# Optimization experiments

Measured on AMD Instinct MI355X. Metric: run time of the kernel, lower is better.

Reference implementation:

```python
import jax, jax.numpy as jnp
import numpy as np

B, N_C, Y_DIM = 8, 2048, 8
GRID_RES = 128
GRID_MIN, GRID_MAX = -1.0, 1.0
SIGMA0 = 0.1


def _make_grid_points():
    x = jnp.linspace(GRID_MIN, GRID_MAX, GRID_RES, dtype=jnp.float32)
    y = jnp.linspace(GRID_MIN, GRID_MAX, GRID_RES, dtype=jnp.float32)
    gy, gx = jnp.meshgrid(y, x, indexing='ij')
    return jnp.stack([gx, gy], axis=-1).reshape(1, -1, 2)  # (1, R*R, 2)


def setup_inputs() -> dict:
    key = jax.random.key(0)
    k1, k2 = jax.random.split(key)
    x_c = jax.random.uniform(k1, (B, N_C, 2), dtype=jnp.float32, minval=GRID_MIN, maxval=GRID_MAX)
    y_c = jax.random.normal(k2, (B, N_C, Y_DIM), dtype=jnp.float32)
    grid_points = _make_grid_points()
    sigma = jnp.asarray(SIGMA0, dtype=jnp.float32)
    return {"x_c": x_c, "y_c": y_c, "grid_points": grid_points, "sigma": sigma}


def reference(x_c, y_c, grid_points, sigma):
    g = grid_points[0]                                    # (M, 2)
    xn = jnp.sum(x_c * x_c, axis=-1)                      # (B, N)
    gn = jnp.sum(g * g, axis=-1)                          # (M,)
    cross = jnp.einsum('bnd,md->bnm', x_c, g)             # (B, N, M)
    d2 = xn[:, :, None] + gn[None, None, :] - 2.0 * cross # (B, N, M)
    weights = jnp.exp(-0.5 * d2 / (sigma * sigma))        # (B, N, M)
    density = jnp.sum(weights, axis=1)                    # (B, M)
    signal = jnp.einsum('bny,bnm->bym', y_c, weights)     # (B, Y, M)
    normalized = signal / (density[:, None, :] + 1e-5)
    out = jnp.concatenate([density[:, None, :], normalized], axis=1)  # (B, 1+Y, M)
    return out.reshape(x_c.shape[0], -1, GRID_RES, GRID_RES)
```

## Files before the change

### kernel.cpp

```cpp
#include <hip/hip_runtime.h>


typedef float  f32x4 __attribute__((ext_vector_type(4)));
typedef __fp16 half8  __attribute__((ext_vector_type(8)));
typedef __fp16 half2t __attribute__((ext_vector_type(2)));

constexpr int B_  = 8;
constexpr int NC  = 2048;
constexpr int M_  = 128 * 128;
constexpr int BLK = 1024;
constexpr int KW  = 128;
constexpr int LDHY = NC + 8;

constexpr int OFF_SXT = 0;
constexpr int OFF_SYT = OFF_SXT + NC * 4;
constexpr int OFF_SYS = OFF_SYT + NC * 4;
constexpr int OFF_SG  = OFF_SYS + 8 * LDHY * 2;
constexpr int SLOT_F  = 2 * 9 * 256;
constexpr int POOL_B  = 8 * SLOT_F * 4;

__global__ __launch_bounds__(BLK) void rbf_sep(
    const float* __restrict__ x_c,
    const float* __restrict__ y_c,
    const float* __restrict__ gp,
    const float* __restrict__ sigma_p,
    float* __restrict__ out)
{
    __shared__ __align__(16) char pool[POOL_B];
    float*  sxt = (float*)(pool + OFF_SXT);
    float*  syt = (float*)(pool + OFF_SYT);
    __fp16* sys = (__fp16*)(pool + OFF_SYS);
    float*  sg  = (float*)(pool + OFF_SG);

    const int tid  = (int)threadIdx.x;
    const int lane = tid & 63;
    const int w    = tid >> 6;
    const int q    = lane >> 4;
    const int cl   = lane & 15;

    const int bid = blockIdx.x;
    const int b   = bid >> 5;
    const int myg = (bid >> 3) & 3;
    const int mxg = bid & 7;
    const int my0 = myg * 32;
    const int mx0 = mxg * 16;

    const float sigma = sigma_p[0];
    const float s = __builtin_sqrtf(0.72134752044448170f) / sigma;

    if (tid < 32)      sg[tid] = s * gp[(my0 + tid) * 256 + 1];
    else if (tid < 48) sg[tid] = s * gp[(mx0 + (tid - 32)) * 2];

    const float2* xb = (const float2*)x_c + (size_t)b * NC;
    const float4* yb = (const float4*)y_c + (size_t)b * NC * 2;
    for (int it = tid; it < NC; it += BLK) {
        const float2 v = xb[it];
        sxt[it] = s * v.x;
        syt[it] = s * v.y;
        const float4 y0 = yb[(size_t)it * 2];
        const float4 y1 = yb[(size_t)it * 2 + 1];
        __fp16* yw = sys + it;
        yw[0 * LDHY] = (__fp16)y0.x;
        yw[1 * LDHY] = (__fp16)y0.y;
        yw[2 * LDHY] = (__fp16)y0.z;
        yw[3 * LDHY] = (__fp16)y0.w;
        yw[4 * LDHY] = (__fp16)y1.x;
        yw[5 * LDHY] = (__fp16)y1.y;
        yw[6 * LDHY] = (__fp16)y1.z;
        yw[7 * LDHY] = (__fp16)y1.w;
    }
    __syncthreads();

    const float sgy0 = sg[cl];
    const float sgy1 = sg[16 + cl];
    const float sgxr = sg[32 + cl];

    f32x4 acc[2][9];
#pragma unroll
    for (int t = 0; t < 2; ++t)
#pragma unroll
        for (int c = 0; c < 9; ++c) acc[t][c] = (f32x4)0.0f;

    const int kbase = w * KW;
#pragma unroll 2
    for (int ks = 0; ks < KW / 32; ++ks) {
        const int kq = kbase + ks * 32 + q * 8;

        const f32x4 ya0 = *(const f32x4*)(syt + kq);
        const f32x4 ya1 = *(const f32x4*)(syt + kq + 4);
        const f32x4 xa0 = *(const f32x4*)(sxt + kq);
        const f32x4 xa1 = *(const f32x4*)(sxt + kq + 4);

        const f32x4 y0e0 = ya0 - sgy0, y0e1 = ya1 - sgy0;
        const f32x4 y0m0 = y0e0 * y0e0, y0m1 = y0e1 * y0e1;
        const half2t p00 = __builtin_amdgcn_cvt_pkrtz(
            __builtin_amdgcn_exp2f(-y0m0.x), __builtin_amdgcn_exp2f(-y0m0.y));
        const half2t p01 = __builtin_amdgcn_cvt_pkrtz(
            __builtin_amdgcn_exp2f(-y0m0.z), __builtin_amdgcn_exp2f(-y0m0.w));
        const half2t p02 = __builtin_amdgcn_cvt_pkrtz(
            __builtin_amdgcn_exp2f(-y0m1.x), __builtin_amdgcn_exp2f(-y0m1.y));
        const half2t p03 = __builtin_amdgcn_cvt_pkrtz(
            __builtin_amdgcn_exp2f(-y0m1.z), __builtin_amdgcn_exp2f(-y0m1.w));
        const half8 af0 = (half8){p00.x, p00.y, p01.x, p01.y, p02.x, p02.y, p03.x, p03.y};

        const f32x4 y1e0 = ya0 - sgy1, y1e1 = ya1 - sgy1;
        const f32x4 y1m0 = y1e0 * y1e0, y1m1 = y1e1 * y1e1;
        const half2t p10 = __builtin_amdgcn_cvt_pkrtz(
            __builtin_amdgcn_exp2f(-y1m0.x), __builtin_amdgcn_exp2f(-y1m0.y));
        const half2t p11 = __builtin_amdgcn_cvt_pkrtz(
            __builtin_amdgcn_exp2f(-y1m0.z), __builtin_amdgcn_exp2f(-y1m0.w));
        const half2t p12 = __builtin_amdgcn_cvt_pkrtz(
            __builtin_amdgcn_exp2f(-y1m1.x), __builtin_amdgcn_exp2f(-y1m1.y));
        const half2t p13 = __builtin_amdgcn_cvt_pkrtz(
            __builtin_amdgcn_exp2f(-y1m1.z), __builtin_amdgcn_exp2f(-y1m1.w));
        const half8 af1 = (half8){p10.x, p10.y, p11.x, p11.y, p12.x, p12.y, p13.x, p13.y};

        const f32x4 xe0 = xa0 - sgxr, xe1 = xa1 - sgxr;
        const f32x4 xm0 = xe0 * xe0,   xm1 = xe1 * xe1;
        const half2t b0 = __builtin_amdgcn_cvt_pkrtz(
            __builtin_amdgcn_exp2f(-xm0.x), __builtin_amdgcn_exp2f(-xm0.y));
        const half2t b1 = __builtin_amdgcn_cvt_pkrtz(
            __builtin_amdgcn_exp2f(-xm0.z), __builtin_amdgcn_exp2f(-xm0.w));
        const half2t b2 = __builtin_amdgcn_cvt_pkrtz(
            __builtin_amdgcn_exp2f(-xm1.x), __builtin_amdgcn_exp2f(-xm1.y));
        const half2t b3 = __builtin_amdgcn_cvt_pkrtz(
            __builtin_amdgcn_exp2f(-xm1.z), __builtin_amdgcn_exp2f(-xm1.w));
        const half8 bx = (half8){b0.x, b0.y, b1.x, b1.y, b2.x, b2.y, b3.x, b3.y};

        acc[0][0] = __builtin_amdgcn_mfma_f32_16x16x32_f16(af0, bx, acc[0][0], 0, 0, 0);
        acc[1][0] = __builtin_amdgcn_mfma_f32_16x16x32_f16(af1, bx, acc[1][0], 0, 0, 0);
        const __fp16* yp = sys + kq;
#pragma unroll
        for (int c = 0; c < 8; ++c) {
            const half8 yf  = *(const half8*)(yp + c * LDHY);
            const half8 bxy = bx * yf;
            acc[0][c + 1] = __builtin_amdgcn_mfma_f32_16x16x32_f16(af0, bxy, acc[0][c + 1], 0, 0, 0);
            acc[1][c + 1] = __builtin_amdgcn_mfma_f32_16x16x32_f16(af1, bxy, acc[1][c + 1], 0, 0, 0);
        }
    }

    __syncthreads();
    float* slots = (float*)pool;
    if (w >= 8) {
        float* rb = slots + (w - 8) * SLOT_F;
#pragma unroll
        for (int t = 0; t < 2; ++t)
#pragma unroll
            for (int c = 0; c < 9; ++c)
#pragma unroll
                for (int r = 0; r < 4; ++r)
                    rb[t * 2304 + c * 256 + (q * 4 + r) * 16 + cl] = acc[t][c][r];
    }
    __syncthreads();
    if (w < 8) {
        float* rb = slots + w * SLOT_F;
#pragma unroll
        for (int t = 0; t < 2; ++t)
#pragma unroll
            for (int c = 0; c < 9; ++c)
#pragma unroll
                for (int r = 0; r < 4; ++r) {
                    const int idx = t * 2304 + c * 256 + (q * 4 + r) * 16 + cl;
                    rb[idx] = rb[idx] + acc[t][c][r];
                }
    }
    __syncthreads();

    float* ob = out + (size_t)b * 9 * M_;
    for (int it = tid; it < 1152; it += BLK) {
        const int t  = it / 576;
        const int rr = it % 576;
        const int c  = rr >> 6;
        const int my = (rr & 63) >> 2;
        const int xq = rr & 3;
        const int base  = t * 2304 + c * 256 + my * 16 + xq * 4;
        const int dbase = t * 2304 +           my * 16 + xq * 4;

        #define SUM8(off) ( (*(const f32x4*)(slots + 0*SLOT_F + (off)) + *(const f32x4*)(slots + 1*SLOT_F + (off))) \
                          + (*(const f32x4*)(slots + 2*SLOT_F + (off)) + *(const f32x4*)(slots + 3*SLOT_F + (off))) \
                          + ((*(const f32x4*)(slots + 4*SLOT_F + (off)) + *(const f32x4*)(slots + 5*SLOT_F + (off))) \
                          +  (*(const f32x4*)(slots + 6*SLOT_F + (off)) + *(const f32x4*)(slots + 7*SLOT_F + (off)))) )
        const f32x4 v = SUM8(base);
        f32x4 o;
        if (c == 0) {
            o = v;
        } else {
            const f32x4 d = SUM8(dbase);
            o.x = v.x * __builtin_amdgcn_rcpf(d.x + 1e-5f);
            o.y = v.y * __builtin_amdgcn_rcpf(d.y + 1e-5f);
            o.z = v.z * __builtin_amdgcn_rcpf(d.z + 1e-5f);
            o.w = v.w * __builtin_amdgcn_rcpf(d.w + 1e-5f);
        }
        #undef SUM8
        *(f32x4*)(ob + (size_t)c * M_ + (size_t)(my0 + t * 16 + my) * 128 + mx0 + xq * 4) = o;
    }
}

extern "C" void kernel_launch(void* const* d_in, const int* in_sizes, int n_in,
                              void* d_out, int out_size, void* d_ws, size_t ws_size,
                              hipStream_t stream) {
    const float* x_c   = (const float*)d_in[0];
    const float* y_c   = (const float*)d_in[1];
    const float* gp    = (const float*)d_in[2];
    const float* sigma = (const float*)d_in[3];
    float* out = (float*)d_out;

    dim3 grid(B_ * 32);
    dim3 block(BLK);
    rbf_sep<<<grid, block, 0, stream>>>(x_c, y_c, gp, sigma, out);
}
```

Measured before the change: 17.92 us.

## Halve block to 512 threads with two blocks per CU and simplify epilogue

The block shrinks from 16 to 8 waves. Each wave now covers 256 of the K points instead of 128, and the launch bounds ask for 2 blocks per CU. The cross-wave reduction uses 4 shared slots instead of 8, which halves shared memory and lets two blocks be co-resident to overlap one block's prologue and epilogue with another's compute. The final epilogue has each thread own one grid point, sum 4 slots and compute the reciprocal of the density once, then do scalar stores instead of vectorized f32x4 stores.

```diff
diff --git a/kernel.cpp b/kernel.cpp
--- a/kernel.cpp
+++ b/kernel.cpp
@@ -8,8 +8,8 @@
 constexpr int B_  = 8;
 constexpr int NC  = 2048;
 constexpr int M_  = 128 * 128;
-constexpr int BLK = 1024;
-constexpr int KW  = 128;
+constexpr int BLK = 512;
+constexpr int KW  = 256;
 constexpr int LDHY = NC + 8;
 
 constexpr int OFF_SXT = 0;
@@ -17,9 +17,9 @@
 constexpr int OFF_SYS = OFF_SYT + NC * 4;
 constexpr int OFF_SG  = OFF_SYS + 8 * LDHY * 2;
 constexpr int SLOT_F  = 2 * 9 * 256;
-constexpr int POOL_B  = 8 * SLOT_F * 4;
-
-__global__ __launch_bounds__(BLK) void rbf_sep(
+constexpr int POOL_B  = 4 * SLOT_F * 4;
+
+__global__ __launch_bounds__(BLK, 2) void rbf_sep(
     const float* __restrict__ x_c,
     const float* __restrict__ y_c,
     const float* __restrict__ gp,
@@ -141,8 +141,8 @@
 
     __syncthreads();
     float* slots = (float*)pool;
-    if (w >= 8) {
-        float* rb = slots + (w - 8) * SLOT_F;
+    if (w >= 4) {
+        float* rb = slots + (w - 4) * SLOT_F;
 #pragma unroll
         for (int t = 0; t < 2; ++t)
 #pragma unroll
@@ -152,7 +152,7 @@
                     rb[t * 2304 + c * 256 + (q * 4 + r) * 16 + cl] = acc[t][c][r];
     }
     __syncthreads();
-    if (w < 8) {
+    if (w < 4) {
         float* rb = slots + w * SLOT_F;
 #pragma unroll
         for (int t = 0; t < 2; ++t)
@@ -166,33 +166,24 @@
     }
     __syncthreads();
 
-    float* ob = out + (size_t)b * 9 * M_;
-    for (int it = tid; it < 1152; it += BLK) {
-        const int t  = it / 576;
-        const int rr = it % 576;
-        const int c  = rr >> 6;
-        const int my = (rr & 63) >> 2;
-        const int xq = rr & 3;
-        const int base  = t * 2304 + c * 256 + my * 16 + xq * 4;
-        const int dbase = t * 2304 +           my * 16 + xq * 4;
-
-        #define SUM8(off) ( (*(const f32x4*)(slots + 0*SLOT_F + (off)) + *(const f32x4*)(slots + 1*SLOT_F + (off))) \
-                          + (*(const f32x4*)(slots + 2*SLOT_F + (off)) + *(const f32x4*)(slots + 3*SLOT_F + (off))) \
-                          + ((*(const f32x4*)(slots + 4*SLOT_F + (off)) + *(const f32x4*)(slots + 5*SLOT_F + (off))) \
-                          +  (*(const f32x4*)(slots + 6*SLOT_F + (off)) + *(const f32x4*)(slots + 7*SLOT_F + (off)))) )
-        const f32x4 v = SUM8(base);
-        f32x4 o;
-        if (c == 0) {
-            o = v;
-        } else {
-            const f32x4 d = SUM8(dbase);
-            o.x = v.x * __builtin_amdgcn_rcpf(d.x + 1e-5f);
-            o.y = v.y * __builtin_amdgcn_rcpf(d.y + 1e-5f);
-            o.z = v.z * __builtin_amdgcn_rcpf(d.z + 1e-5f);
-            o.w = v.w * __builtin_amdgcn_rcpf(d.w + 1e-5f);
+    {
+        float* ob = out + (size_t)b * 9 * M_;
+        const int t  = tid >> 8;
+        const int my = (tid >> 4) & 15;
+        const int mx = tid & 15;
+        const size_t mo = (size_t)(my0 + t * 16 + my) * 128 + mx0 + mx;
+        float v[9];
+#pragma unroll
+        for (int c = 0; c < 9; ++c) {
+            const int idx = t * 2304 + c * 256 + my * 16 + mx;
+            v[c] = (slots[idx] + slots[SLOT_F + idx]) +
+                   (slots[2 * SLOT_F + idx] + slots[3 * SLOT_F + idx]);
         }
-        #undef SUM8
-        *(f32x4*)(ob + (size_t)c * M_ + (size_t)(my0 + t * 16 + my) * 128 + mx0 + xq * 4) = o;
+        const float inv = __builtin_amdgcn_rcpf(v[0] + 1e-5f);
+        ob[mo] = v[0];
+#pragma unroll
+        for (int c = 1; c < 9; ++c)
+            ob[(size_t)c * M_ + mo] = v[c] * inv;
     }
 }
 
```

Result: faster. 16.80 us (-6.2%).
